# Optimization experiments

Hardware: AMD Instinct MI355X
Metric: run time of the kernel (lower is better)

The kernel has to match this reference:

```python
import jax, jax.numpy as jnp
import numpy as np

N_NODES = 50000
N_EDGES = 800000
D_FEAT = 128
UNITS = 128


def setup_inputs() -> dict:
    key = jax.random.key(0)
    k1, k2, k3, k4, k5 = jax.random.split(key, 5)
    node_states = jax.random.normal(k1, (N_NODES, D_FEAT), dtype=jnp.float32)
    src = jnp.sort(jax.random.randint(k2, (N_EDGES,), 0, N_NODES))
    dst = jax.random.randint(k3, (N_EDGES,), 0, N_NODES)
    edges = jnp.stack([src, dst], axis=1).astype(jnp.int64)  # [E,2], sorted by source
    kernel = jax.random.normal(k4, (D_FEAT, UNITS), dtype=jnp.float32) * (1.0 / np.sqrt(D_FEAT))
    kernel_attention = jax.random.normal(k5, (2 * UNITS, 1), dtype=jnp.float32) * (1.0 / np.sqrt(2 * UNITS))
    return {"node_states": node_states, "edges": edges, "kernel": kernel, "kernel_attention": kernel_attention}


def reference(node_states, edges, kernel, kernel_attention):
    n_nodes = node_states.shape[0]
    src, dst = edges[:, 0], edges[:, 1]
    # linear transform of node features
    h = node_states @ kernel                                  # [N, U]
    # per-edge concatenated (src, dst) features -> raw attention logit
    e_feat = jnp.concatenate([h[src], h[dst]], axis=-1)       # [E, 2U]
    logits = jax.nn.leaky_relu((e_feat @ kernel_attention)[:, 0], negative_slope=0.2)  # [E]
    scores = jnp.exp(jnp.clip(logits, -2.0, 2.0))             # [E]
    # segment softmax over incoming edges of each source node
    denom = jax.ops.segment_sum(scores, src, num_segments=n_nodes)  # [N]
    alpha = scores / denom[src]                                # [E]
    # weighted aggregation of neighbor features
    out = jax.ops.segment_sum(h[dst] * alpha[:, None], src, num_segments=n_nodes)  # [N, U]
    return out
```

## Files before the change

kernel.cpp:

```cpp
#include <hip/hip_runtime.h>

#define N_NODES 50000
#define N_EDGES 800000
#define D 128
#define TM 128

__device__ __forceinline__ unsigned short f2bf(float f) {
    union { float f; unsigned u; } v; v.f = f;
    return (unsigned short)((v.u + 0x7fffu + ((v.u >> 16) & 1u)) >> 16);
}
__device__ __forceinline__ float bflo(unsigned u) {
    union { unsigned u; float f; } c; c.u = u << 16; return c.f;
}
__device__ __forceinline__ float bfhi(unsigned u) {
    union { unsigned u; float f; } c; c.u = u & 0xffff0000u; return c.f;
}

__global__ void k1_rowptr(const int* __restrict__ edges, int* __restrict__ row_ptr) {
    int n = blockIdx.x * blockDim.x + threadIdx.x;
    if (n > N_NODES) return;
    int lo = 0, hi = N_EDGES;
    while (lo < hi) {
        int mid = (lo + hi) >> 1;
        if (edges[2 * mid] < n) lo = mid + 1; else hi = mid;
    }
    row_ptr[n] = lo;
}

__global__ __launch_bounds__(256) void kh(const float* __restrict__ X,
                                          const float* __restrict__ W,
                                          const float* __restrict__ ka,
                                          unsigned short* __restrict__ h,
                                          float* __restrict__ a_src,
                                          float* __restrict__ a_dst,
                                          int n_rows) {
    __shared__ float As[TM * D];
    __shared__ float kas[2 * D];
    int tid = threadIdx.x;
    int row0 = blockIdx.x * TM;

    kas[tid] = ka[tid];
    for (int i = tid; i < TM * D / 4; i += 256) {
        int r = i >> 5;
        int gr = row0 + r;
        float4 v = make_float4(0.f, 0.f, 0.f, 0.f);
        if (gr < n_rows) v = ((const float4*)(X + (size_t)gr * D))[i & 31];
        ((float4*)As)[i] = v;
    }
    __syncthreads();

    int cg = tid & 15;
    int rg = tid >> 4;
    int c0 = cg * 8;
    int r0 = rg * 8;
    float acc[8][8];
#pragma unroll
    for (int i = 0; i < 8; ++i)
#pragma unroll
        for (int j = 0; j < 8; ++j) acc[i][j] = 0.f;

    for (int k = 0; k < D; k += 4) {
        float4 av[8];
#pragma unroll
        for (int i = 0; i < 8; ++i)
            av[i] = *(const float4*)&As[(r0 + i) * D + k];
#pragma unroll
        for (int kk = 0; kk < 4; ++kk) {
            float4 wlo = *(const float4*)(W + (k + kk) * D + c0);
            float4 whi = *(const float4*)(W + (k + kk) * D + c0 + 4);
            float wv[8] = {wlo.x, wlo.y, wlo.z, wlo.w, whi.x, whi.y, whi.z, whi.w};
#pragma unroll
            for (int i = 0; i < 8; ++i) {
                float a = (kk == 0) ? av[i].x : (kk == 1) ? av[i].y
                        : (kk == 2) ? av[i].z : av[i].w;
#pragma unroll
                for (int j = 0; j < 8; ++j) acc[i][j] += a * wv[j];
            }
        }
    }

#pragma unroll
    for (int i = 0; i < 8; ++i) {
        int row = row0 + r0 + i;
        float ps = 0.f, pd = 0.f;
#pragma unroll
        for (int j = 0; j < 8; ++j) {
            ps += acc[i][j] * kas[c0 + j];
            pd += acc[i][j] * kas[D + c0 + j];
        }
        for (int off = 8; off > 0; off >>= 1) {
            ps += __shfl_down(ps, off, 16);
            pd += __shfl_down(pd, off, 16);
        }
        if (row < n_rows) {
            union { unsigned short us[8]; uint4 q; } pk;
#pragma unroll
            for (int j = 0; j < 8; ++j) pk.us[j] = f2bf(acc[i][j]);
            *(uint4*)&h[(size_t)row * D + c0] = pk.q;
            if (cg == 0) { a_src[row] = ps; a_dst[row] = pd; }
        }
    }
}

__global__ __launch_bounds__(256) void k3(const int* __restrict__ edges,
                                          const int* __restrict__ row_ptr,
                                          const unsigned short* __restrict__ h,
                                          const float* __restrict__ a_src,
                                          const float* __restrict__ a_dst,
                                          float* __restrict__ out) {
    int node = blockIdx.x * 4 + (threadIdx.x >> 6);
    if (node >= N_NODES) return;
    int lane = threadIdx.x & 63;
    int q = lane >> 4;
    int l16 = lane & 15;

    int start = row_ptr[node], end = row_ptr[node + 1];
    float asn = a_src[node];

    float4 accA = make_float4(0.f, 0.f, 0.f, 0.f);
    float4 accB = make_float4(0.f, 0.f, 0.f, 0.f);
    float dn = 0.f;

    for (int base = start; base < end; base += 64) {
        int cnt = min(64, end - base);
        int d = 0; float s = 0.f;
        if (lane < cnt) {
            d = edges[2 * (base + lane) + 1];
            float lg = asn + a_dst[d];
            lg = (lg >= 0.f) ? lg : 0.2f * lg;
            lg = fminf(fmaxf(lg, -2.f), 2.f);
            s = __expf(lg);
        }
        for (int j = 0; j < cnt; j += 4) {
            int slot = j + q;
            float sj = __shfl(s, slot, 64);
            int   dj = __shfl(d, slot, 64);
            uint4 p = *(const uint4*)(h + ((size_t)dj << 7) + (l16 << 3));
            accA.x += sj * bflo(p.x); accA.y += sj * bfhi(p.x);
            accA.z += sj * bflo(p.y); accA.w += sj * bfhi(p.y);
            accB.x += sj * bflo(p.z); accB.y += sj * bfhi(p.z);
            accB.z += sj * bflo(p.w); accB.w += sj * bfhi(p.w);
            dn += sj;
        }
    }

    float vals[9] = {accA.x, accA.y, accA.z, accA.w,
                     accB.x, accB.y, accB.z, accB.w, dn};
#pragma unroll
    for (int m = 32; m >= 16; m >>= 1)
#pragma unroll
        for (int i = 0; i < 9; ++i) vals[i] += __shfl_xor(vals[i], m, 64);

    if (q == 0) {
        float inv = (end > start) ? 1.f / vals[8] : 0.f;
        float4 o0 = make_float4(vals[0] * inv, vals[1] * inv, vals[2] * inv, vals[3] * inv);
        float4 o1 = make_float4(vals[4] * inv, vals[5] * inv, vals[6] * inv, vals[7] * inv);
        float* op = out + (size_t)node * D + l16 * 8;
        *(float4*)op = o0;
        *(float4*)(op + 4) = o1;
    }
}

extern "C" void kernel_launch(void* const* d_in, const int* in_sizes, int n_in,
                              void* d_out, int out_size, void* d_ws, size_t ws_size,
                              hipStream_t stream) {
    const float* X     = (const float*)d_in[0];
    const int*   edges = (const int*)d_in[1];
    const float* W     = (const float*)d_in[2];
    const float* ka    = (const float*)d_in[3];

    char* ws = (char*)d_ws;
    unsigned short* h = (unsigned short*)ws;
    float* a_src   = (float*)(ws + (size_t)N_NODES * D * 2);
    float* a_dst   = a_src + N_NODES;
    int*   row_ptr = (int*)(a_dst + N_NODES);
    float* out = (float*)d_out;

    k1_rowptr<<<(N_NODES + 1 + 255) / 256, 256, 0, stream>>>(edges, row_ptr);
    kh<<<(N_NODES + TM - 1) / TM, 256, 0, stream>>>(X, W, ka, h, a_src, a_dst, N_NODES);
    k3<<<(N_NODES + 3) / 4, 256, 0, stream>>>(edges, row_ptr, h, a_src, a_dst, out);
}
```

Baseline: 151.3 us.

## Use bf16 MFMA for projection GEMM and fold attention vector into W

The FP32 scalar GEMM for h = X·W is replaced by bf16 MFMA 16x16x32 instructions. W is transposed to bf16 in a prep kernel that also does the row_ptr binary search. Attention logits are now computed directly from X using precomputed u = W·ka_src and v = W·ka_dst, and the gather loop is unrolled by two to issue more loads in flight. In exchange, X is quantized to bf16 before the matmul, which lowers precision, and h is written with scattered 2-byte stores.

```diff
diff --git a/kernel.cpp b/kernel.cpp
--- a/kernel.cpp
+++ b/kernel.cpp
@@ -3,7 +3,10 @@
 #define N_NODES 50000
 #define N_EDGES 800000
 #define D 128
-#define TM 128
+#define LDA 136
+
+typedef __attribute__((ext_vector_type(8))) short bf16x8;
+typedef __attribute__((ext_vector_type(4))) float f32x4;
 
 __device__ __forceinline__ unsigned short f2bf(float f) {
     union { float f; unsigned u; } v; v.f = f;
@@ -16,89 +19,111 @@
     union { unsigned u; float f; } c; c.u = u & 0xffff0000u; return c.f;
 }
 
-__global__ void k1_rowptr(const int* __restrict__ edges, int* __restrict__ row_ptr) {
-    int n = blockIdx.x * blockDim.x + threadIdx.x;
-    if (n > N_NODES) return;
-    int lo = 0, hi = N_EDGES;
-    while (lo < hi) {
-        int mid = (lo + hi) >> 1;
-        if (edges[2 * mid] < n) lo = mid + 1; else hi = mid;
-    }
-    row_ptr[n] = lo;
+#define NB_SEARCH 196
+__global__ void k1_prep(const int* __restrict__ edges, const float* __restrict__ W,
+                        const float* __restrict__ ka, int* __restrict__ row_ptr,
+                        unsigned short* __restrict__ Wt,
+                        float* __restrict__ u, float* __restrict__ v) {
+    int b = blockIdx.x, tid = threadIdx.x;
+    if (b < NB_SEARCH) {
+        int n = b * 256 + tid;
+        if (n > N_NODES) return;
+        int lo = 0, hi = N_EDGES;
+        while (lo < hi) {
+            int mid = (lo + hi) >> 1;
+            if (edges[2 * mid] < n) lo = mid + 1; else hi = mid;
+        }
+        row_ptr[n] = lo;
+    } else if (b < NB_SEARCH + 8) {
+        int bi = b - NB_SEARCH;
+        for (int i = tid; i < 16 * D; i += 256) {
+            int n = bi * 16 + (i >> 7), k = i & 127;
+            Wt[n * D + k] = f2bf(W[k * D + n]);
+        }
+    } else {
+        int k = tid & 127;
+        const float* kap = ka + ((tid >> 7) ? D : 0);
+        float s = 0.f;
+        for (int j = 0; j < D; ++j) s += W[k * D + j] * kap[j];
+        if (tid < 128) u[k] = s; else v[k] = s;
+    }
 }
 
 __global__ __launch_bounds__(256) void kh(const float* __restrict__ X,
-                                          const float* __restrict__ W,
-                                          const float* __restrict__ ka,
+                                          const unsigned short* __restrict__ Wt,
+                                          const float* __restrict__ u,
+                                          const float* __restrict__ v,
                                           unsigned short* __restrict__ h,
                                           float* __restrict__ a_src,
-                                          float* __restrict__ a_dst,
-                                          int n_rows) {
-    __shared__ float As[TM * D];
-    __shared__ float kas[2 * D];
+                                          float* __restrict__ a_dst) {
+    __shared__ unsigned short As[128 * LDA];
+    __shared__ unsigned short Bs[128 * LDA];
     int tid = threadIdx.x;
-    int row0 = blockIdx.x * TM;
-
-    kas[tid] = ka[tid];
-    for (int i = tid; i < TM * D / 4; i += 256) {
-        int r = i >> 5;
+    int row0 = blockIdx.x * 128;
+
+    for (int i = tid; i < 2048; i += 256) {
+        int r = i >> 4, c = i & 15;
+        *(uint4*)&Bs[r * LDA + c * 8] = *(const uint4*)&Wt[r * D + c * 8];
+    }
+    for (int i = tid; i < 2048; i += 256) {
+        int r = i >> 4, c = i & 15;
         int gr = row0 + r;
-        float4 v = make_float4(0.f, 0.f, 0.f, 0.f);
-        if (gr < n_rows) v = ((const float4*)(X + (size_t)gr * D))[i & 31];
-        ((float4*)As)[i] = v;
+        union { unsigned short us[8]; uint4 q; } pk;
+        if (gr < N_NODES) {
+            const float* xp = X + (size_t)gr * D + c * 8;
+#pragma unroll
+            for (int j = 0; j < 8; ++j) pk.us[j] = f2bf(xp[j]);
+        } else pk.q = make_uint4(0u, 0u, 0u, 0u);
+        *(uint4*)&As[r * LDA + c * 8] = pk.q;
     }
     __syncthreads();
 
-    int cg = tid & 15;
-    int rg = tid >> 4;
-    int c0 = cg * 8;
-    int r0 = rg * 8;
-    float acc[8][8];
-#pragma unroll
-    for (int i = 0; i < 8; ++i)
-#pragma unroll
-        for (int j = 0; j < 8; ++j) acc[i][j] = 0.f;
-
-    for (int k = 0; k < D; k += 4) {
-        float4 av[8];
-#pragma unroll
-        for (int i = 0; i < 8; ++i)
-            av[i] = *(const float4*)&As[(r0 + i) * D + k];
-#pragma unroll
-        for (int kk = 0; kk < 4; ++kk) {
-            float4 wlo = *(const float4*)(W + (k + kk) * D + c0);
-            float4 whi = *(const float4*)(W + (k + kk) * D + c0 + 4);
-            float wv[8] = {wlo.x, wlo.y, wlo.z, wlo.w, whi.x, whi.y, whi.z, whi.w};
-#pragma unroll
-            for (int i = 0; i < 8; ++i) {
-                float a = (kk == 0) ? av[i].x : (kk == 1) ? av[i].y
-                        : (kk == 2) ? av[i].z : av[i].w;
-#pragma unroll
-                for (int j = 0; j < 8; ++j) acc[i][j] += a * wv[j];
+    int wave = tid >> 6, lane = tid & 63;
+    int m16 = lane & 15, quad = lane >> 4;
+    int wr0 = wave * 32;
+    f32x4 acc[2][8];
+#pragma unroll
+    for (int i = 0; i < 2; ++i)
+#pragma unroll
+        for (int j = 0; j < 8; ++j) acc[i][j] = (f32x4){0.f, 0.f, 0.f, 0.f};
+
+    for (int k0 = 0; k0 < D; k0 += 32) {
+        bf16x8 a0 = *(const bf16x8*)&As[(wr0 + m16) * LDA + k0 + quad * 8];
+        bf16x8 a1 = *(const bf16x8*)&As[(wr0 + 16 + m16) * LDA + k0 + quad * 8];
+#pragma unroll
+        for (int j = 0; j < 8; ++j) {
+            bf16x8 bf = *(const bf16x8*)&Bs[(j * 16 + m16) * LDA + k0 + quad * 8];
+            acc[0][j] = __builtin_amdgcn_mfma_f32_16x16x32_bf16(a0, bf, acc[0][j], 0, 0, 0);
+            acc[1][j] = __builtin_amdgcn_mfma_f32_16x16x32_bf16(a1, bf, acc[1][j], 0, 0, 0);
+        }
+    }
+
+#pragma unroll
+    for (int i = 0; i < 2; ++i)
+#pragma unroll
+        for (int j = 0; j < 8; ++j)
+#pragma unroll
+            for (int r = 0; r < 4; ++r) {
+                int row = row0 + wr0 + i * 16 + quad * 4 + r;
+                if (row < N_NODES)
+                    h[(size_t)row * D + j * 16 + m16] = f2bf(acc[i][j][r]);
             }
-        }
-    }
-
-#pragma unroll
-    for (int i = 0; i < 8; ++i) {
-        int row = row0 + r0 + i;
+
+    int rr = tid >> 1, hf = tid & 1;
+    int grow = row0 + rr;
+    if (grow < N_NODES) {
+        const float* xp = X + (size_t)grow * D + hf * 64;
         float ps = 0.f, pd = 0.f;
-#pragma unroll
-        for (int j = 0; j < 8; ++j) {
-            ps += acc[i][j] * kas[c0 + j];
-            pd += acc[i][j] * kas[D + c0 + j];
-        }
-        for (int off = 8; off > 0; off >>= 1) {
-            ps += __shfl_down(ps, off, 16);
-            pd += __shfl_down(pd, off, 16);
-        }
-        if (row < n_rows) {
-            union { unsigned short us[8]; uint4 q; } pk;
-#pragma unroll
-            for (int j = 0; j < 8; ++j) pk.us[j] = f2bf(acc[i][j]);
-            *(uint4*)&h[(size_t)row * D + c0] = pk.q;
-            if (cg == 0) { a_src[row] = ps; a_dst[row] = pd; }
-        }
+        for (int jj = 0; jj < 64; jj += 4) {
+            float4 xv = *(const float4*)(xp + jj);
+            float4 uv = *(const float4*)(u + hf * 64 + jj);
+            float4 vv = *(const float4*)(v + hf * 64 + jj);
+            ps += xv.x * uv.x + xv.y * uv.y + xv.z * uv.z + xv.w * uv.w;
+            pd += xv.x * vv.x + xv.y * vv.y + xv.z * vv.z + xv.w * vv.w;
+        }
+        ps += __shfl_xor(ps, 1, 64);
+        pd += __shfl_xor(pd, 1, 64);
+        if (hf == 0) { a_src[grow] = ps; a_dst[grow] = pd; }
     }
 }
 
@@ -131,16 +156,22 @@
             lg = fminf(fmaxf(lg, -2.f), 2.f);
             s = __expf(lg);
         }
-        for (int j = 0; j < cnt; j += 4) {
-            int slot = j + q;
-            float sj = __shfl(s, slot, 64);
-            int   dj = __shfl(d, slot, 64);
-            uint4 p = *(const uint4*)(h + ((size_t)dj << 7) + (l16 << 3));
-            accA.x += sj * bflo(p.x); accA.y += sj * bfhi(p.x);
-            accA.z += sj * bflo(p.y); accA.w += sj * bfhi(p.y);
-            accB.x += sj * bflo(p.z); accB.y += sj * bfhi(p.z);
-            accB.z += sj * bflo(p.w); accB.w += sj * bfhi(p.w);
-            dn += sj;
+        for (int j = 0; j < cnt; j += 8) {
+            float s0 = __shfl(s, j + q, 64);
+            int   d0 = __shfl(d, j + q, 64);
+            float s1 = __shfl(s, j + q + 4, 64);
+            int   d1 = __shfl(d, j + q + 4, 64);
+            uint4 p0 = *(const uint4*)(h + ((size_t)d0 << 7) + (l16 << 3));
+            uint4 p1 = *(const uint4*)(h + ((size_t)d1 << 7) + (l16 << 3));
+            accA.x += s0 * bflo(p0.x); accA.y += s0 * bfhi(p0.x);
+            accA.z += s0 * bflo(p0.y); accA.w += s0 * bfhi(p0.y);
+            accB.x += s0 * bflo(p0.z); accB.y += s0 * bfhi(p0.z);
+            accB.z += s0 * bflo(p0.w); accB.w += s0 * bfhi(p0.w);
+            accA.x += s1 * bflo(p1.x); accA.y += s1 * bfhi(p1.x);
+            accA.z += s1 * bflo(p1.y); accA.w += s1 * bfhi(p1.y);
+            accB.x += s1 * bflo(p1.z); accB.y += s1 * bfhi(p1.z);
+            accB.z += s1 * bflo(p1.w); accB.w += s1 * bfhi(p1.w);
+            dn += s0 + s1;
         }
     }
 
@@ -170,13 +201,16 @@
     const float* ka    = (const float*)d_in[3];
 
     char* ws = (char*)d_ws;
-    unsigned short* h = (unsigned short*)ws;
+    unsigned short* h  = (unsigned short*)ws;
     float* a_src   = (float*)(ws + (size_t)N_NODES * D * 2);
     float* a_dst   = a_src + N_NODES;
     int*   row_ptr = (int*)(a_dst + N_NODES);
+    unsigned short* Wt = (unsigned short*)(row_ptr + N_NODES + 4);
+    float* u = (float*)(Wt + D * D);
+    float* v = u + D;
     float* out = (float*)d_out;
 
-    k1_rowptr<<<(N_NODES + 1 + 255) / 256, 256, 0, stream>>>(edges, row_ptr);
-    kh<<<(N_NODES + TM - 1) / TM, 256, 0, stream>>>(X, W, ka, h, a_src, a_dst, N_NODES);
+    k1_prep<<<NB_SEARCH + 9, 256, 0, stream>>>(edges, W, ka, row_ptr, Wt, u, v);
+    kh<<<(N_NODES + 127) / 128, 256, 0, stream>>>(X, Wt, u, v, h, a_src, a_dst);
     k3<<<(N_NODES + 3) / 4, 256, 0, stream>>>(edges, row_ptr, h, a_src, a_dst, out);
 }
```

Result: faster. 134.3 us (-11.2%).
